# Kernel optimization log

Hardware: AMD Instinct MI355X
Metric: run time of the kernel (lower is better)

Reference implementation:

```python
import jax, jax.numpy as jnp
import numpy as np

B = 65536
OBS_DIM, ACT_DIM = 64, 16
FEAT_DIM = 128
EMB_DIM = 32
N_ENV = 64
HID = 256
IN_DIM = 2 * OBS_DIM + ACT_DIM + 1  # obs, delta_obs, act, rew
LEAKY_SLOPE = 0.01


def setup_inputs() -> dict:
    key = jax.random.key(0)
    ks = jax.random.split(key, 16)
    def lin(kw, kb, fan_in, fan_out):
        bound = 1.0 / np.sqrt(fan_in)
        W = jax.random.uniform(kw, (fan_in, fan_out), jnp.float32, -bound, bound)
        b = jax.random.uniform(kb, (fan_out,), jnp.float32, -bound, bound)
        return W, b
    W0, b0 = lin(ks[0], ks[1], IN_DIM, HID)
    W1, b1 = lin(ks[2], ks[3], HID, HID)
    W2, b2 = lin(ks[4], ks[5], HID, FEAT_DIM)
    return {
        "obs": jax.random.normal(ks[6], (B, OBS_DIM), jnp.float32),
        "act": jax.random.normal(ks[7], (B, ACT_DIM), jnp.float32),
        "obs2": jax.random.normal(ks[8], (B, OBS_DIM), jnp.float32),
        "rew": jax.random.normal(ks[9], (B, 1), jnp.float32),
        "W0": W0, "b0": b0, "W1": W1, "b1": b1, "W2": W2, "b2": b2,
        # per-env projection W ~ N(0, 0.05) as in torch.normal(zeros, 0.05)
        "W_proj": 0.05 * jax.random.normal(ks[10], (N_ENV, EMB_DIM, FEAT_DIM), jnp.float32),
        # running-mean embedding buffer e (here m * N with N=1, so N(0,1))
        "e_emb": jax.random.normal(ks[11], (N_ENV, EMB_DIM), jnp.float32),
        # learnable length scale, initialized to length_scale=1.0
        "sigma": jnp.ones((N_ENV,), jnp.float32),
    }


def reference(obs, act, obs2, rew, W0, b0, W1, b1, W2, b2, W_proj, e_emb, sigma):
    # ---- E_Encoder.compute_feature: MLP with LeakyReLU (incl. output activation)
    x = jnp.concatenate([obs, obs2 - obs, act, rew], axis=-1)  # (B, IN_DIM)
    h = jax.nn.leaky_relu(x @ W0 + b0, LEAKY_SLOPE)
    h = jax.nn.leaky_relu(h @ W1 + b1, LEAKY_SLOPE)
    feature = jax.nn.leaky_relu(h @ W2 + b2, LEAKY_SLOPE)  # (B, FEAT_DIM)
    # ---- calc_embedding: per-env projection
    f2e = jnp.einsum('bf,nef->bne', feature, W_proj)  # (B, N_ENV, EMB_DIM)
    # ---- RBF distance
    diff = f2e - e_emb[None]  # (B, N_ENV, EMB_DIM)
    distance = jnp.exp(-jnp.mean(diff * diff, axis=-1) / (2.0 * sigma * sigma))  # (B, N_ENV)
    # ---- inference (id=None branch): argmin + gathers
    idx = jnp.argmin(distance, axis=1)  # (B,)
    chosen_mean = e_emb[idx]  # (B, EMB_DIM)
    chosen_embedding = jnp.take_along_axis(f2e, idx[:, None, None], axis=1)[:, 0, :]  # (B, EMB_DIM)
    chosen_dist = jnp.take_along_axis(distance, idx[:, None], axis=1)  # (B, 1)
    return chosen_embedding, chosen_dist, idx[:, None], chosen_mean, distance
```

## Files before the change

### kernel.cpp

```cpp
#include <hip/hip_runtime.h>
#include <hip/hip_bf16.h>

#define B_TOT 65536
#define WPT_FLOATS (64 * 32 * 128)


__global__ __launch_bounds__(256, 2) void udp_mlp(
    const float* __restrict__ obs, const float* __restrict__ act,
    const float* __restrict__ obs2, const float* __restrict__ rew,
    const float* __restrict__ W0, const float* __restrict__ b0,
    const float* __restrict__ W1, const float* __restrict__ b1,
    const float* __restrict__ W2, const float* __restrict__ b2,
    const float* __restrict__ Wp, float* __restrict__ WpT,
    float* __restrict__ out) {
  __shared__ __align__(16) float A_[5120];
  __shared__ __align__(16) float Bb[8192];
  const int t = threadIdx.x;
  const int blockRow = blockIdx.x * 32;

  float* out0 = out;
  float* out3 = out + (size_t)B_TOT * 34;
  float* out4 = out + (size_t)B_TOT * 66;

  if (WpT != nullptr && t < 128) {
    const int idx = blockIdx.x * 128 + t;
    const int j  = idx & 3;
    const int n  = (idx >> 2) & 63;
    const int f4 = (idx >> 8) & 31;
    const int e  = idx >> 13;
    WpT[idx] = Wp[(n * 32 + e) * 128 + f4 * 4 + j];
  }

  for (int i = t; i < 32 * 160; i += 256) {
    int r = i / 160, k = i - r * 160;
    int row = blockRow + r;
    float v;
    if (k < 64)        v = obs[row * 64 + k];
    else if (k < 128)  v = obs2[row * 64 + (k - 64)] - obs[row * 64 + (k - 64)];
    else if (k < 144)  v = act[row * 16 + (k - 128)];
    else if (k == 144) v = rew[row];
    else               v = 0.f;
    A_[i] = v;
  }
  __syncthreads();

  {
    const int n4 = (t & 63) * 4;
    const int rbase = (t >> 6) * 8;
    float aA[8], aB[8], aC[8], aD[8];
#pragma unroll
    for (int r = 0; r < 8; ++r) { aA[r] = 0.f; aB[r] = 0.f; aC[r] = 0.f; aD[r] = 0.f; }
    const float4 bb = *(const float4*)&b0[n4];
    const float4 wt = *(const float4*)&W0[144 * 256 + n4];
    for (int k4 = 0; k4 < 144; k4 += 4) {
      const float4 w0 = *(const float4*)&W0[(k4 + 0) * 256 + n4];
      const float4 w1 = *(const float4*)&W0[(k4 + 1) * 256 + n4];
      const float4 w2 = *(const float4*)&W0[(k4 + 2) * 256 + n4];
      const float4 w3 = *(const float4*)&W0[(k4 + 3) * 256 + n4];
#pragma unroll
      for (int r = 0; r < 8; ++r) {
        const float4 xv = *(const float4*)&A_[(rbase + r) * 160 + k4];
        aA[r] = fmaf(xv.x, w0.x, aA[r]); aA[r] = fmaf(xv.y, w1.x, aA[r]);
        aA[r] = fmaf(xv.z, w2.x, aA[r]); aA[r] = fmaf(xv.w, w3.x, aA[r]);
        aB[r] = fmaf(xv.x, w0.y, aB[r]); aB[r] = fmaf(xv.y, w1.y, aB[r]);
        aB[r] = fmaf(xv.z, w2.y, aB[r]); aB[r] = fmaf(xv.w, w3.y, aB[r]);
        aC[r] = fmaf(xv.x, w0.z, aC[r]); aC[r] = fmaf(xv.y, w1.z, aC[r]);
        aC[r] = fmaf(xv.z, w2.z, aC[r]); aC[r] = fmaf(xv.w, w3.z, aC[r]);
        aD[r] = fmaf(xv.x, w0.w, aD[r]); aD[r] = fmaf(xv.y, w1.w, aD[r]);
        aD[r] = fmaf(xv.z, w2.w, aD[r]); aD[r] = fmaf(xv.w, w3.w, aD[r]);
      }
    }
#pragma unroll
    for (int r = 0; r < 8; ++r) {
      const float xt = A_[(rbase + r) * 160 + 144];
      aA[r] = fmaf(xt, wt.x, aA[r]); aB[r] = fmaf(xt, wt.y, aB[r]);
      aC[r] = fmaf(xt, wt.z, aC[r]); aD[r] = fmaf(xt, wt.w, aD[r]);
    }
#pragma unroll
    for (int r = 0; r < 8; ++r) {
      float4 v;
      v.x = aA[r] + bb.x; v.x = v.x > 0.f ? v.x : 0.01f * v.x;
      v.y = aB[r] + bb.y; v.y = v.y > 0.f ? v.y : 0.01f * v.y;
      v.z = aC[r] + bb.z; v.z = v.z > 0.f ? v.z : 0.01f * v.z;
      v.w = aD[r] + bb.w; v.w = v.w > 0.f ? v.w : 0.01f * v.w;
      *(float4*)&Bb[(rbase + r) * 256 + n4] = v;
    }
  }
  __syncthreads();

  {
    const int n4 = (t & 63) * 4;
    const int rbase = (t >> 6) * 8;
    float aA[8], aB[8], aC[8], aD[8];
#pragma unroll
    for (int r = 0; r < 8; ++r) { aA[r] = 0.f; aB[r] = 0.f; aC[r] = 0.f; aD[r] = 0.f; }
    const float4 bb = *(const float4*)&b1[n4];
    for (int k4 = 0; k4 < 256; k4 += 4) {
      const float4 w0 = *(const float4*)&W1[(k4 + 0) * 256 + n4];
      const float4 w1 = *(const float4*)&W1[(k4 + 1) * 256 + n4];
      const float4 w2 = *(const float4*)&W1[(k4 + 2) * 256 + n4];
      const float4 w3 = *(const float4*)&W1[(k4 + 3) * 256 + n4];
#pragma unroll
      for (int r = 0; r < 8; ++r) {
        const float4 xv = *(const float4*)&Bb[(rbase + r) * 256 + k4];
        aA[r] = fmaf(xv.x, w0.x, aA[r]); aA[r] = fmaf(xv.y, w1.x, aA[r]);
        aA[r] = fmaf(xv.z, w2.x, aA[r]); aA[r] = fmaf(xv.w, w3.x, aA[r]);
        aB[r] = fmaf(xv.x, w0.y, aB[r]); aB[r] = fmaf(xv.y, w1.y, aB[r]);
        aB[r] = fmaf(xv.z, w2.y, aB[r]); aB[r] = fmaf(xv.w, w3.y, aB[r]);
        aC[r] = fmaf(xv.x, w0.z, aC[r]); aC[r] = fmaf(xv.y, w1.z, aC[r]);
        aC[r] = fmaf(xv.z, w2.z, aC[r]); aC[r] = fmaf(xv.w, w3.z, aC[r]);
        aD[r] = fmaf(xv.x, w0.w, aD[r]); aD[r] = fmaf(xv.y, w1.w, aD[r]);
        aD[r] = fmaf(xv.z, w2.w, aD[r]); aD[r] = fmaf(xv.w, w3.w, aD[r]);
      }
    }
    __syncthreads();
#pragma unroll
    for (int r = 0; r < 8; ++r) {
      float4 v;
      v.x = aA[r] + bb.x; v.x = v.x > 0.f ? v.x : 0.01f * v.x;
      v.y = aB[r] + bb.y; v.y = v.y > 0.f ? v.y : 0.01f * v.y;
      v.z = aC[r] + bb.z; v.z = v.z > 0.f ? v.z : 0.01f * v.z;
      v.w = aD[r] + bb.w; v.w = v.w > 0.f ? v.w : 0.01f * v.w;
      *(float4*)&Bb[(rbase + r) * 256 + n4] = v;
    }
  }
  __syncthreads();

  {
    const int n4 = (t & 31) * 4;
    const int rbase = (t >> 5) * 4;
    float aA[4], aB[4], aC[4], aD[4];
#pragma unroll
    for (int r = 0; r < 4; ++r) { aA[r] = 0.f; aB[r] = 0.f; aC[r] = 0.f; aD[r] = 0.f; }
    const float4 bb = *(const float4*)&b2[n4];
    for (int k4 = 0; k4 < 256; k4 += 4) {
      const float4 w0 = *(const float4*)&W2[(k4 + 0) * 128 + n4];
      const float4 w1 = *(const float4*)&W2[(k4 + 1) * 128 + n4];
      const float4 w2 = *(const float4*)&W2[(k4 + 2) * 128 + n4];
      const float4 w3 = *(const float4*)&W2[(k4 + 3) * 128 + n4];
#pragma unroll
      for (int r = 0; r < 4; ++r) {
        const float4 xv = *(const float4*)&Bb[(rbase + r) * 256 + k4];
        aA[r] = fmaf(xv.x, w0.x, aA[r]); aA[r] = fmaf(xv.y, w1.x, aA[r]);
        aA[r] = fmaf(xv.z, w2.x, aA[r]); aA[r] = fmaf(xv.w, w3.x, aA[r]);
        aB[r] = fmaf(xv.x, w0.y, aB[r]); aB[r] = fmaf(xv.y, w1.y, aB[r]);
        aB[r] = fmaf(xv.z, w2.y, aB[r]); aB[r] = fmaf(xv.w, w3.y, aB[r]);
        aC[r] = fmaf(xv.x, w0.z, aC[r]); aC[r] = fmaf(xv.y, w1.z, aC[r]);
        aC[r] = fmaf(xv.z, w2.z, aC[r]); aC[r] = fmaf(xv.w, w3.z, aC[r]);
        aD[r] = fmaf(xv.x, w0.w, aD[r]); aD[r] = fmaf(xv.y, w1.w, aD[r]);
        aD[r] = fmaf(xv.z, w2.w, aD[r]); aD[r] = fmaf(xv.w, w3.w, aD[r]);
      }
    }
#pragma unroll
    for (int r = 0; r < 4; ++r) {
      float4 v;
      v.x = aA[r] + bb.x; v.x = v.x > 0.f ? v.x : 0.01f * v.x;
      v.y = aB[r] + bb.y; v.y = v.y > 0.f ? v.y : 0.01f * v.y;
      v.z = aC[r] + bb.z; v.z = v.z > 0.f ? v.z : 0.01f * v.z;
      v.w = aD[r] + bb.w; v.w = v.w > 0.f ? v.w : 0.01f * v.w;
      const size_t row = (size_t)blockRow + rbase + r;
      if (n4 < 32)      *(float4*)&out0[row * 32 + n4] = v;
      else if (n4 < 64) *(float4*)&out3[row * 32 + (n4 - 32)] = v;
      else              *(float4*)&out4[row * 64 + (n4 - 64)] = v;
    }
  }
}

template <int COAL>
__global__ __launch_bounds__(256, 2) void udp_dist(
    const float* __restrict__ Wp, const float* __restrict__ WpT,
    const float* __restrict__ emb, const float* __restrict__ sigma,
    float* __restrict__ out) {
  __shared__ __align__(16) float A_[8192];
  __shared__ __align__(16) float Bb[4096];
  __shared__ float idxArr[32];
  const int t = threadIdx.x;
  const int blockRow = blockIdx.x * 32;

  float* out0 = out;
  float* out1 = out + (size_t)B_TOT * 32;
  float* out2 = out + (size_t)B_TOT * 33;
  float* out3 = out + (size_t)B_TOT * 34;
  float* out4 = out + (size_t)B_TOT * 66;

  for (int i = t; i < 1024; i += 256) {
    const int r = i >> 5, c4 = (i & 31) * 4;
    const size_t row = (size_t)blockRow + r;
    float4 v;
    if (c4 < 32)      v = *(const float4*)&out0[row * 32 + c4];
    else if (c4 < 64) v = *(const float4*)&out3[row * 32 + (c4 - 32)];
    else              v = *(const float4*)&out4[row * 64 + (c4 - 64)];
    *(float4*)&Bb[r * 128 + c4] = v;
  }
  __syncthreads();

  {
    const int n = t & 63, pp = t >> 6;
    const float* eb = emb + n * 32;
#pragma unroll 1
    for (int q = 0; q < 2; ++q) {
      const int rbase = q * 16;
      float rj0[16], rj1[16];
#pragma unroll
      for (int r = 0; r < 16; ++r) { rj0[r] = 0.f; rj1[r] = 0.f; }
#pragma unroll 1
      for (int mm = 0; mm < 2; ++mm) {
        const int e00 = 2 * pp + 16 * mm;
        const int e01 = e00 + 1;
        const int e10 = e00 + 8;
        const int e11 = e00 + 9;
        const float *p00, *p01, *p10, *p11;
        if (COAL) {
          p00 = WpT + e00 * 8192 + n * 4;
          p01 = WpT + e01 * 8192 + n * 4;
          p10 = WpT + e10 * 8192 + n * 4;
          p11 = WpT + e11 * 8192 + n * 4;
        } else {
          p00 = Wp + ((size_t)n * 32 + e00) * 128;
          p01 = Wp + ((size_t)n * 32 + e01) * 128;
          p10 = Wp + ((size_t)n * 32 + e10) * 128;
          p11 = Wp + ((size_t)n * 32 + e11) * 128;
        }
        const int WSTR = COAL ? 256 : 4;
        float a00[16], a01[16], a10[16], a11[16];
#pragma unroll
        for (int r = 0; r < 16; ++r) { a00[r] = 0.f; a01[r] = 0.f; a10[r] = 0.f; a11[r] = 0.f; }
        for (int ff = 0; ff < 32; ++ff) {
          const float4 w00 = *(const float4*)(p00 + ff * WSTR);
          const float4 w01 = *(const float4*)(p01 + ff * WSTR);
          const float4 w10 = *(const float4*)(p10 + ff * WSTR);
          const float4 w11 = *(const float4*)(p11 + ff * WSTR);
#pragma unroll
          for (int r = 0; r < 16; ++r) {
            const float4 fv = *(const float4*)&Bb[(rbase + r) * 128 + ff * 4];
            a00[r] = fmaf(fv.x, w00.x, a00[r]);
            a00[r] = fmaf(fv.y, w00.y, a00[r]);
            a00[r] = fmaf(fv.z, w00.z, a00[r]);
            a00[r] = fmaf(fv.w, w00.w, a00[r]);
            a01[r] = fmaf(fv.x, w01.x, a01[r]);
            a01[r] = fmaf(fv.y, w01.y, a01[r]);
            a01[r] = fmaf(fv.z, w01.z, a01[r]);
            a01[r] = fmaf(fv.w, w01.w, a01[r]);
            a10[r] = fmaf(fv.x, w10.x, a10[r]);
            a10[r] = fmaf(fv.y, w10.y, a10[r]);
            a10[r] = fmaf(fv.z, w10.z, a10[r]);
            a10[r] = fmaf(fv.w, w10.w, a10[r]);
            a11[r] = fmaf(fv.x, w11.x, a11[r]);
            a11[r] = fmaf(fv.y, w11.y, a11[r]);
            a11[r] = fmaf(fv.z, w11.z, a11[r]);
            a11[r] = fmaf(fv.w, w11.w, a11[r]);
          }
        }
        const float em00 = eb[e00], em01 = eb[e01];
        const float em10 = eb[e10], em11 = eb[e11];
#pragma unroll
        for (int r = 0; r < 16; ++r) {
          float d;
          d = a00[r] - em00; rj0[r] = fmaf(d, d, rj0[r]);
          d = a01[r] - em01; rj1[r] = fmaf(d, d, rj1[r]);
          d = a10[r] - em10; rj0[r] = fmaf(d, d, rj0[r]);
          d = a11[r] - em11; rj1[r] = fmaf(d, d, rj1[r]);
        }
      }
#pragma unroll
      for (int r = 0; r < 16; ++r) {
        const int gr = rbase + r;
        A_[gr * 256 + pp * 64 + ((n + gr) & 63)] = rj0[r] + rj1[r];
      }
    }
  }
  __syncthreads();

  {
    const int r = t >> 3, k = t & 7;
    float best = 1e30f;
    int bi = 0;
    for (int u = 0; u < 8; ++u) {
      const int nn = 8 * k + u;
      const int nr = (nn + r) & 63;
      const float p0 = A_[r * 256 + 0 * 64 + nr];
      const float p1 = A_[r * 256 + 1 * 64 + nr];
      const float p2 = A_[r * 256 + 2 * 64 + nr];
      const float p3 = A_[r * 256 + 3 * 64 + nr];
      float s = (p0 + p1) + (p2 + p3);
      float mean = s / 32.0f;
      float sg = sigma[nn];
      float den = 2.0f * sg * sg;
      float dist = expf((-mean) / den);
      A_[r * 256 + nr] = dist;
      if (dist < best) { best = dist; bi = nn; }
    }
#pragma unroll
    for (int m = 1; m < 8; m <<= 1) {
      const float ob = __shfl_xor(best, m);
      const int obi = __shfl_xor(bi, m);
      if (ob < best || (ob == best && obi < bi)) { best = ob; bi = obi; }
    }
    if (k == 0) {
      const size_t row = (size_t)blockRow + r;
      idxArr[r] = (float)bi;
      out1[row] = best;
      out2[row] = (float)bi;
    }
  }
  __syncthreads();

  for (int i = t; i < 32 * 64; i += 256) {
    int r = i >> 6, n = i & 63;
    out4[(size_t)(blockRow + r) * 64 + n] = A_[r * 256 + ((n + r) & 63)];
  }
  for (int i = t; i < 32 * 32; i += 256) {
    int r = i >> 5, e = i & 31;
    int bi = (int)idxArr[r];
    const float* wrow = Wp + (bi * 32 + e) * 128;
    float acc = 0.f;
    for (int f4 = 0; f4 < 128; f4 += 4) {
      const float4 wv = *(const float4*)(wrow + f4);
      const float4 fv = *(const float4*)&Bb[r * 128 + f4];
      acc = fmaf(fv.x, wv.x, acc);
      acc = fmaf(fv.y, wv.y, acc);
      acc = fmaf(fv.z, wv.z, acc);
      acc = fmaf(fv.w, wv.w, acc);
    }
    size_t row = (size_t)blockRow + r;
    out0[row * 32 + e] = acc;
    out3[row * 32 + e] = emb[bi * 32 + e];
  }
}

extern "C" void kernel_launch(void* const* d_in, const int* in_sizes, int n_in,
                              void* d_out, int out_size, void* d_ws, size_t ws_size,
                              hipStream_t stream) {
  const float* obs   = (const float*)d_in[0];
  const float* act   = (const float*)d_in[1];
  const float* obs2  = (const float*)d_in[2];
  const float* rew   = (const float*)d_in[3];
  const float* W0    = (const float*)d_in[4];
  const float* b0    = (const float*)d_in[5];
  const float* W1    = (const float*)d_in[6];
  const float* b1    = (const float*)d_in[7];
  const float* W2    = (const float*)d_in[8];
  const float* b2    = (const float*)d_in[9];
  const float* Wp    = (const float*)d_in[10];
  const float* e_emb = (const float*)d_in[11];
  const float* sigma = (const float*)d_in[12];

  const bool coal = (d_ws != nullptr) && (ws_size >= WPT_FLOATS * sizeof(float));
  float* WpT = coal ? (float*)d_ws : nullptr;

  udp_mlp<<<dim3(B_TOT / 32), dim3(256), 0, stream>>>(
      obs, act, obs2, rew, W0, b0, W1, b1, W2, b2, Wp, WpT, (float*)d_out);
  if (coal) {
    udp_dist<1><<<dim3(B_TOT / 32), dim3(256), 0, stream>>>(
        Wp, WpT, e_emb, sigma, (float*)d_out);
  } else {
    udp_dist<0><<<dim3(B_TOT / 32), dim3(256), 0, stream>>>(
        Wp, Wp, e_emb, sigma, (float*)d_out);
  }
}
```

Baseline: 848.3 us.

## Process distance kernel in 16-row halves to shrink shared memory footprint

Restructures the distance kernel so each 16-row half of the 32-row block loads features, computes projections, finalizes distances/argmin, and writes outputs before moving to the next half. Shared memory drops from about 48KB to about 24KB, which may allow more resident blocks per CU and better latency hiding. In exchange it adds extra barriers per half and leaves half the threads idle during the argmin phase.

```diff
diff --git a/kernel.cpp b/kernel.cpp
--- a/kernel.cpp
+++ b/kernel.cpp
@@ -171,9 +171,9 @@
     const float* __restrict__ Wp, const float* __restrict__ WpT,
     const float* __restrict__ emb, const float* __restrict__ sigma,
     float* __restrict__ out) {
-  __shared__ __align__(16) float A_[8192];
-  __shared__ __align__(16) float Bb[4096];
-  __shared__ float idxArr[32];
+  __shared__ __align__(16) float Fb[2048];
+  __shared__ __align__(16) float P_[4096];
+  __shared__ float idxArr[16];
   const int t = threadIdx.x;
   const int blockRow = blockIdx.x * 32;
 
@@ -183,23 +183,25 @@
   float* out3 = out + (size_t)B_TOT * 34;
   float* out4 = out + (size_t)B_TOT * 66;
 
-  for (int i = t; i < 1024; i += 256) {
-    const int r = i >> 5, c4 = (i & 31) * 4;
-    const size_t row = (size_t)blockRow + r;
-    float4 v;
-    if (c4 < 32)      v = *(const float4*)&out0[row * 32 + c4];
-    else if (c4 < 64) v = *(const float4*)&out3[row * 32 + (c4 - 32)];
-    else              v = *(const float4*)&out4[row * 64 + (c4 - 64)];
-    *(float4*)&Bb[r * 128 + c4] = v;
-  }
-  __syncthreads();
-
-  {
-    const int n = t & 63, pp = t >> 6;
-    const float* eb = emb + n * 32;
+  const int n = t & 63, pp = t >> 6;
+  const float* eb = emb + n * 32;
+
 #pragma unroll 1
-    for (int q = 0; q < 2; ++q) {
-      const int rbase = q * 16;
+  for (int q = 0; q < 2; ++q) {
+    const int rbase = q * 16;
+
+    for (int i = t; i < 512; i += 256) {
+      const int r = i >> 5, c4 = (i & 31) * 4;
+      const size_t row = (size_t)blockRow + rbase + r;
+      float4 v;
+      if (c4 < 32)      v = *(const float4*)&out0[row * 32 + c4];
+      else if (c4 < 64) v = *(const float4*)&out3[row * 32 + (c4 - 32)];
+      else              v = *(const float4*)&out4[row * 64 + (c4 - 64)];
+      *(float4*)&Fb[r * 128 + c4] = v;
+    }
+    __syncthreads();
+
+    {
       float rj0[16], rj1[16];
 #pragma unroll
       for (int r = 0; r < 16; ++r) { rj0[r] = 0.f; rj1[r] = 0.f; }
@@ -232,7 +234,7 @@
           const float4 w11 = *(const float4*)(p11 + ff * WSTR);
 #pragma unroll
           for (int r = 0; r < 16; ++r) {
-            const float4 fv = *(const float4*)&Bb[(rbase + r) * 128 + ff * 4];
+            const float4 fv = *(const float4*)&Fb[r * 128 + ff * 4];
             a00[r] = fmaf(fv.x, w00.x, a00[r]);
             a00[r] = fmaf(fv.y, w00.y, a00[r]);
             a00[r] = fmaf(fv.z, w00.z, a00[r]);
@@ -265,66 +267,69 @@
 #pragma unroll
       for (int r = 0; r < 16; ++r) {
         const int gr = rbase + r;
-        A_[gr * 256 + pp * 64 + ((n + gr) & 63)] = rj0[r] + rj1[r];
-      }
-    }
-  }
-  __syncthreads();
-
-  {
-    const int r = t >> 3, k = t & 7;
-    float best = 1e30f;
-    int bi = 0;
-    for (int u = 0; u < 8; ++u) {
-      const int nn = 8 * k + u;
-      const int nr = (nn + r) & 63;
-      const float p0 = A_[r * 256 + 0 * 64 + nr];
-      const float p1 = A_[r * 256 + 1 * 64 + nr];
-      const float p2 = A_[r * 256 + 2 * 64 + nr];
-      const float p3 = A_[r * 256 + 3 * 64 + nr];
-      float s = (p0 + p1) + (p2 + p3);
-      float mean = s / 32.0f;
-      float sg = sigma[nn];
-      float den = 2.0f * sg * sg;
-      float dist = expf((-mean) / den);
-      A_[r * 256 + nr] = dist;
-      if (dist < best) { best = dist; bi = nn; }
-    }
-#pragma unroll
-    for (int m = 1; m < 8; m <<= 1) {
-      const float ob = __shfl_xor(best, m);
-      const int obi = __shfl_xor(bi, m);
-      if (ob < best || (ob == best && obi < bi)) { best = ob; bi = obi; }
-    }
-    if (k == 0) {
-      const size_t row = (size_t)blockRow + r;
-      idxArr[r] = (float)bi;
-      out1[row] = best;
-      out2[row] = (float)bi;
-    }
-  }
-  __syncthreads();
-
-  for (int i = t; i < 32 * 64; i += 256) {
-    int r = i >> 6, n = i & 63;
-    out4[(size_t)(blockRow + r) * 64 + n] = A_[r * 256 + ((n + r) & 63)];
-  }
-  for (int i = t; i < 32 * 32; i += 256) {
-    int r = i >> 5, e = i & 31;
-    int bi = (int)idxArr[r];
-    const float* wrow = Wp + (bi * 32 + e) * 128;
-    float acc = 0.f;
-    for (int f4 = 0; f4 < 128; f4 += 4) {
-      const float4 wv = *(const float4*)(wrow + f4);
-      const float4 fv = *(const float4*)&Bb[r * 128 + f4];
-      acc = fmaf(fv.x, wv.x, acc);
-      acc = fmaf(fv.y, wv.y, acc);
-      acc = fmaf(fv.z, wv.z, acc);
-      acc = fmaf(fv.w, wv.w, acc);
-    }
-    size_t row = (size_t)blockRow + r;
-    out0[row * 32 + e] = acc;
-    out3[row * 32 + e] = emb[bi * 32 + e];
+        P_[r * 256 + pp * 64 + ((n + gr) & 63)] = rj0[r] + rj1[r];
+      }
+    }
+    __syncthreads();
+
+    if (t < 128) {
+      const int r = t >> 3, k = t & 7;
+      const int gr = rbase + r;
+      float best = 1e30f;
+      int bi = 0;
+      for (int u = 0; u < 8; ++u) {
+        const int nn = 8 * k + u;
+        const int nr = (nn + gr) & 63;
+        const float p0 = P_[r * 256 + 0 * 64 + nr];
+        const float p1 = P_[r * 256 + 1 * 64 + nr];
+        const float p2 = P_[r * 256 + 2 * 64 + nr];
+        const float p3 = P_[r * 256 + 3 * 64 + nr];
+        float s = (p0 + p1) + (p2 + p3);
+        float mean = s / 32.0f;
+        float sg = sigma[nn];
+        float den = 2.0f * sg * sg;
+        float dist = expf((-mean) / den);
+        P_[r * 256 + nr] = dist;
+        if (dist < best) { best = dist; bi = nn; }
+      }
+#pragma unroll
+      for (int m = 1; m < 8; m <<= 1) {
+        const float ob = __shfl_xor(best, m);
+        const int obi = __shfl_xor(bi, m);
+        if (ob < best || (ob == best && obi < bi)) { best = ob; bi = obi; }
+      }
+      if (k == 0) {
+        const size_t row = (size_t)blockRow + gr;
+        idxArr[r] = (float)bi;
+        out1[row] = best;
+        out2[row] = (float)bi;
+      }
+    }
+    __syncthreads();
+
+    for (int i = t; i < 1024; i += 256) {
+      const int r = i >> 6, nn = i & 63;
+      const int gr = rbase + r;
+      out4[(size_t)(blockRow + gr) * 64 + nn] = P_[r * 256 + ((nn + gr) & 63)];
+    }
+    for (int i = t; i < 512; i += 256) {
+      const int r = i >> 5, e = i & 31;
+      const int bi = (int)idxArr[r];
+      const float* wrow = Wp + (bi * 32 + e) * 128;
+      float acc = 0.f;
+      for (int f4 = 0; f4 < 128; f4 += 4) {
+        const float4 wv = *(const float4*)(wrow + f4);
+        const float4 fv = *(const float4*)&Fb[r * 128 + f4];
+        acc = fmaf(fv.x, wv.x, acc);
+        acc = fmaf(fv.y, wv.y, acc);
+        acc = fmaf(fv.z, wv.z, acc);
+        acc = fmaf(fv.w, wv.w, acc);
+      }
+      const size_t row = (size_t)blockRow + rbase + r;
+      out0[row * 32 + e] = acc;
+      out3[row * 32 + e] = emb[bi * 32 + e];
+    }
+    __syncthreads();
   }
 }
 
```

Result: faster. 823.6 us (-2.9%).

## Fuse MLP and distance kernels, keep features in shared memory

Applied to the files above, without the earlier changes.

Merges the MLP kernel and the RBF distance/argmin kernel into one kernel. The feature tile stays in LDS instead of being written to the output buffer and read back, and the Wp transpose moves into a small separate kernel that runs first. This removes a global round trip of the features and one large launch, but the fused kernel carries both phases' register pressure and shared-memory footprint, which may lower occupancy.

```diff
diff --git a/kernel.cpp b/kernel.cpp
--- a/kernel.cpp
+++ b/kernel.cpp
@@ -5,31 +5,37 @@
 #define WPT_FLOATS (64 * 32 * 128)
 
 
-__global__ __launch_bounds__(256, 2) void udp_mlp(
+__global__ __launch_bounds__(256) void wp_transpose(
+    const float* __restrict__ Wp, float* __restrict__ WpT) {
+  const int idx = blockIdx.x * 256 + threadIdx.x;
+  const int j  = idx & 3;
+  const int n  = (idx >> 2) & 63;
+  const int f4 = (idx >> 8) & 31;
+  const int e  = idx >> 13;
+  WpT[idx] = Wp[(n * 32 + e) * 128 + f4 * 4 + j];
+}
+
+template <int COAL>
+__global__ __launch_bounds__(256, 2) void udp_fused(
     const float* __restrict__ obs, const float* __restrict__ act,
     const float* __restrict__ obs2, const float* __restrict__ rew,
     const float* __restrict__ W0, const float* __restrict__ b0,
     const float* __restrict__ W1, const float* __restrict__ b1,
     const float* __restrict__ W2, const float* __restrict__ b2,
-    const float* __restrict__ Wp, float* __restrict__ WpT,
+    const float* __restrict__ Wp, const float* __restrict__ WpT,
+    const float* __restrict__ emb, const float* __restrict__ sigma,
     float* __restrict__ out) {
   __shared__ __align__(16) float A_[5120];
   __shared__ __align__(16) float Bb[8192];
+  __shared__ float idxArr[32];
   const int t = threadIdx.x;
   const int blockRow = blockIdx.x * 32;
 
   float* out0 = out;
+  float* out1 = out + (size_t)B_TOT * 32;
+  float* out2 = out + (size_t)B_TOT * 33;
   float* out3 = out + (size_t)B_TOT * 34;
   float* out4 = out + (size_t)B_TOT * 66;
-
-  if (WpT != nullptr && t < 128) {
-    const int idx = blockIdx.x * 128 + t;
-    const int j  = idx & 3;
-    const int n  = (idx >> 2) & 63;
-    const int f4 = (idx >> 8) & 31;
-    const int e  = idx >> 13;
-    WpT[idx] = Wp[(n * 32 + e) * 128 + f4 * 4 + j];
-  }
 
   for (int i = t; i < 32 * 160; i += 256) {
     int r = i / 160, k = i - r * 160;
@@ -158,39 +164,8 @@
       v.y = aB[r] + bb.y; v.y = v.y > 0.f ? v.y : 0.01f * v.y;
       v.z = aC[r] + bb.z; v.z = v.z > 0.f ? v.z : 0.01f * v.z;
       v.w = aD[r] + bb.w; v.w = v.w > 0.f ? v.w : 0.01f * v.w;
-      const size_t row = (size_t)blockRow + rbase + r;
-      if (n4 < 32)      *(float4*)&out0[row * 32 + n4] = v;
-      else if (n4 < 64) *(float4*)&out3[row * 32 + (n4 - 32)] = v;
-      else              *(float4*)&out4[row * 64 + (n4 - 64)] = v;
-    }
-  }
-}
-
-template <int COAL>
-__global__ __launch_bounds__(256, 2) void udp_dist(
-    const float* __restrict__ Wp, const float* __restrict__ WpT,
-    const float* __restrict__ emb, const float* __restrict__ sigma,
-    float* __restrict__ out) {
-  __shared__ __align__(16) float A_[8192];
-  __shared__ __align__(16) float Bb[4096];
-  __shared__ float idxArr[32];
-  const int t = threadIdx.x;
-  const int blockRow = blockIdx.x * 32;
-
-  float* out0 = out;
-  float* out1 = out + (size_t)B_TOT * 32;
-  float* out2 = out + (size_t)B_TOT * 33;
-  float* out3 = out + (size_t)B_TOT * 34;
-  float* out4 = out + (size_t)B_TOT * 66;
-
-  for (int i = t; i < 1024; i += 256) {
-    const int r = i >> 5, c4 = (i & 31) * 4;
-    const size_t row = (size_t)blockRow + r;
-    float4 v;
-    if (c4 < 32)      v = *(const float4*)&out0[row * 32 + c4];
-    else if (c4 < 64) v = *(const float4*)&out3[row * 32 + (c4 - 32)];
-    else              v = *(const float4*)&out4[row * 64 + (c4 - 64)];
-    *(float4*)&Bb[r * 128 + c4] = v;
+      *(float4*)&A_[(rbase + r) * 128 + n4] = v;
+    }
   }
   __syncthreads();
 
@@ -232,7 +207,7 @@
           const float4 w11 = *(const float4*)(p11 + ff * WSTR);
 #pragma unroll
           for (int r = 0; r < 16; ++r) {
-            const float4 fv = *(const float4*)&Bb[(rbase + r) * 128 + ff * 4];
+            const float4 fv = *(const float4*)&A_[(rbase + r) * 128 + ff * 4];
             a00[r] = fmaf(fv.x, w00.x, a00[r]);
             a00[r] = fmaf(fv.y, w00.y, a00[r]);
             a00[r] = fmaf(fv.z, w00.z, a00[r]);
@@ -265,7 +240,7 @@
 #pragma unroll
       for (int r = 0; r < 16; ++r) {
         const int gr = rbase + r;
-        A_[gr * 256 + pp * 64 + ((n + gr) & 63)] = rj0[r] + rj1[r];
+        Bb[gr * 256 + pp * 64 + ((n + gr) & 63)] = rj0[r] + rj1[r];
       }
     }
   }
@@ -278,16 +253,16 @@
     for (int u = 0; u < 8; ++u) {
       const int nn = 8 * k + u;
       const int nr = (nn + r) & 63;
-      const float p0 = A_[r * 256 + 0 * 64 + nr];
-      const float p1 = A_[r * 256 + 1 * 64 + nr];
-      const float p2 = A_[r * 256 + 2 * 64 + nr];
-      const float p3 = A_[r * 256 + 3 * 64 + nr];
+      const float p0 = Bb[r * 256 + 0 * 64 + nr];
+      const float p1 = Bb[r * 256 + 1 * 64 + nr];
+      const float p2 = Bb[r * 256 + 2 * 64 + nr];
+      const float p3 = Bb[r * 256 + 3 * 64 + nr];
       float s = (p0 + p1) + (p2 + p3);
       float mean = s / 32.0f;
       float sg = sigma[nn];
       float den = 2.0f * sg * sg;
       float dist = expf((-mean) / den);
-      A_[r * 256 + nr] = dist;
+      Bb[r * 256 + nr] = dist;
       if (dist < best) { best = dist; bi = nn; }
     }
 #pragma unroll
@@ -306,8 +281,8 @@
   __syncthreads();
 
   for (int i = t; i < 32 * 64; i += 256) {
-    int r = i >> 6, n = i & 63;
-    out4[(size_t)(blockRow + r) * 64 + n] = A_[r * 256 + ((n + r) & 63)];
+    int r = i >> 6, nn = i & 63;
+    out4[(size_t)(blockRow + r) * 64 + nn] = Bb[r * 256 + ((nn + r) & 63)];
   }
   for (int i = t; i < 32 * 32; i += 256) {
     int r = i >> 5, e = i & 31;
@@ -316,7 +291,7 @@
     float acc = 0.f;
     for (int f4 = 0; f4 < 128; f4 += 4) {
       const float4 wv = *(const float4*)(wrow + f4);
-      const float4 fv = *(const float4*)&Bb[r * 128 + f4];
+      const float4 fv = *(const float4*)&A_[r * 128 + f4];
       acc = fmaf(fv.x, wv.x, acc);
       acc = fmaf(fv.y, wv.y, acc);
       acc = fmaf(fv.z, wv.z, acc);
@@ -348,13 +323,14 @@
   const bool coal = (d_ws != nullptr) && (ws_size >= WPT_FLOATS * sizeof(float));
   float* WpT = coal ? (float*)d_ws : nullptr;
 
-  udp_mlp<<<dim3(B_TOT / 32), dim3(256), 0, stream>>>(
-      obs, act, obs2, rew, W0, b0, W1, b1, W2, b2, Wp, WpT, (float*)d_out);
   if (coal) {
-    udp_dist<1><<<dim3(B_TOT / 32), dim3(256), 0, stream>>>(
-        Wp, WpT, e_emb, sigma, (float*)d_out);
+    wp_transpose<<<dim3(WPT_FLOATS / 256), dim3(256), 0, stream>>>(Wp, WpT);
+    udp_fused<1><<<dim3(B_TOT / 32), dim3(256), 0, stream>>>(
+        obs, act, obs2, rew, W0, b0, W1, b1, W2, b2, Wp, WpT, e_emb, sigma,
+        (float*)d_out);
   } else {
-    udp_dist<0><<<dim3(B_TOT / 32), dim3(256), 0, stream>>>(
-        Wp, Wp, e_emb, sigma, (float*)d_out);
+    udp_fused<0><<<dim3(B_TOT / 32), dim3(256), 0, stream>>>(
+        obs, act, obs2, rew, W0, b0, W1, b1, W2, b2, Wp, Wp, e_emb, sigma,
+        (float*)d_out);
   }
 }
```

New measurement: 841.5 us. No clear change (-0.8%).
